# Kernel optimization log

Measured on AMD Instinct MI355X. Metric: run time of the kernel, lower is better.

Reference implementation:

```python
import jax, jax.numpy as jnp
import numpy as np

RATIO = 128        # compress_ratio (coff=1, no overlap)
HEAD_DIM = 512
RD = 64            # rope_head_dim
BLOCK_SIZE = 8192  # token block size of paged KV cache
ENTRIES = 64       # entries per compressed-cache block (BLOCK_SIZE // RATIO)
NUM_BLOCKS = 4     # physical blocks in the paged cache
EPS = 1e-6


def setup_inputs() -> dict:
    key = jax.random.key(0)
    ks = jax.random.split(key, 6)
    B, S, D = 2, 8192, 4096
    x = jax.random.normal(ks[0], (B, S, D), jnp.float32)
    wkv = jax.random.normal(ks[1], (D, HEAD_DIM), jnp.float32) * 0.02
    wgate = jax.random.normal(ks[2], (D, HEAD_DIM), jnp.float32) * 0.02
    ape = jax.random.normal(ks[3], (RATIO, HEAD_DIM), jnp.float32)
    norm_weight = jnp.ones((HEAD_DIM,), jnp.float32)
    # rotary tables for positions 0..S-1 over RD//2 frequencies
    inv_freq = 1.0 / (10000.0 ** (jnp.arange(0, RD, 2, dtype=jnp.float32) / RD))
    ang = jnp.arange(S, dtype=jnp.float32)[:, None] * inv_freq[None, :]
    cos, sin = jnp.cos(ang), jnp.sin(ang)
    # one physical block per sequence (prefill from start_pos=0)
    block_offsets = jnp.arange(B, dtype=jnp.int32).reshape(B, 1)
    return {"x": x, "wkv": wkv, "wgate": wgate, "ape": ape,
            "norm_weight": norm_weight, "cos": cos, "sin": sin,
            "block_offsets": block_offsets}


def reference(x, wkv, wgate, ape, norm_weight, cos, sin, block_offsets):
    B, S, D = x.shape
    NC = S // RATIO  # compressed tokens per sequence
    # projections, then reshape into compression windows of RATIO tokens
    kv = jnp.einsum('bsd,dh->bsh', x, wkv).reshape(B, NC, RATIO, HEAD_DIM)
    sc = jnp.einsum('bsd,dh->bsh', x, wgate).reshape(B, NC, RATIO, HEAD_DIM)
    # score_kv: gate scores + absolute-position bias -> softmax over the window,
    # weighted sum pools RATIO tokens into one compressed entry per channel
    w = jax.nn.softmax(sc + ape[None, None], axis=2)        # [B, NC, RATIO, H]
    comp = jnp.sum(w * kv, axis=2)                          # [B, NC, H]
    # RMSNorm (fp32 accumulation)
    ms = jnp.mean(jnp.square(comp.astype(jnp.float32)), axis=-1, keepdims=True)
    comp = (comp.astype(jnp.float32) * jax.lax.rsqrt(ms + EPS)).astype(x.dtype) * norm_weight
    # RoPE on last RD dims at the window-start token position (start_pos+1-ratio)
    pos = jnp.arange(NC) * RATIO                            # [NC]
    c, s = cos[pos], sin[pos]                               # [NC, RD//2]
    rot = comp[..., -RD:].reshape(B, NC, RD // 2, 2)
    rr = rot[..., 0] * c - rot[..., 1] * s
    ri = rot[..., 0] * s + rot[..., 1] * c
    comp = jnp.concatenate(
        [comp[..., :-RD], jnp.stack([rr, ri], axis=-1).reshape(B, NC, RD)], axis=-1)
    # scatter compressed entries into the paged block cache
    cidx = jnp.arange(NC)
    blk = (cidx * RATIO) // BLOCK_SIZE                      # logical block index
    off = cidx % ENTRIES                                    # offset within block
    phys = block_offsets[:, blk].astype(jnp.int32)          # [B, NC]
    cache = jnp.zeros((NUM_BLOCKS, ENTRIES, HEAD_DIM), x.dtype)
    cache = cache.at[phys.reshape(-1), jnp.tile(off, B)].set(comp.reshape(-1, HEAD_DIM))
    return cache
```

## Files before the change

### kernel.cpp

```cpp
#include <hip/hip_runtime.h>
#include <hip/hip_bf16.h>
#include <stdint.h>

typedef __bf16 bf16x8 __attribute__((ext_vector_type(8)));
typedef float f32x4 __attribute__((ext_vector_type(4)));

#define RATIO   128
#define HEADDIM 512
#define RD      64
#define NCW     64
#define BATCH   2
#define SEQ     8192
#define DIM     4096

__device__ __forceinline__ void gload16(const void* g, void* l) {
  __builtin_amdgcn_global_load_lds(
      (__attribute__((address_space(1))) const void*)g,
      (__attribute__((address_space(3))) void*)l, 16, 0, 0);
}

__device__ __forceinline__ __bf16 cvt_bf16(float f) {
  __hip_bfloat16 h = __float2bfloat16(f);
  return *reinterpret_cast<__bf16*>(&h);
}

__global__ __launch_bounds__(256) void prep_weights(
    const float* __restrict__ w0, const float* __restrict__ w1,
    __hip_bfloat16* __restrict__ wTs) {
  __shared__ float tile[64][132];
  const int wsel = blockIdx.z, hb = blockIdx.y, k0t = blockIdx.x;
  const float* in = wsel ? w1 : w0;
  const int t = threadIdx.x;
  const int h4 = (t & 31) * 4;
  #pragma unroll
  for (int p = 0; p < 8; ++p) {
    const int k = (t >> 5) + p * 8;
    const f32x4 v = *reinterpret_cast<const f32x4*>(
        in + (size_t)(k0t * 64 + k) * HEADDIM + hb * 128 + h4);
    tile[k][h4 + 0] = v[0]; tile[k][h4 + 1] = v[1];
    tile[k][h4 + 2] = v[2]; tile[k][h4 + 3] = v[3];
  }
  __syncthreads();
  const int row = t >> 1;
  __hip_bfloat16* outbase =
      wTs + (((size_t)(wsel * 4 + hb) * 64 + k0t) * 1024 + (size_t)row * 8) * 8;
  #pragma unroll
  for (int q = 0; q < 4; ++q) {
    const int slot = (t & 1) * 4 + q;
    const int kk = (slot ^ (row & 7)) * 8;
    bf16x8 c;
    #pragma unroll
    for (int j = 0; j < 8; ++j) c[j] = cvt_bf16(tile[kk + j][row]);
    *reinterpret_cast<bf16x8*>(outbase + slot * 8) = c;
  }
}

__device__ __forceinline__ bf16x8 ldfrag(const __hip_bfloat16* s, int row, int c16) {
  return *reinterpret_cast<const bf16x8*>(
      reinterpret_cast<const char*>(s) + row * 128 + ((c16 ^ (row & 7)) << 4));
}

__global__ __launch_bounds__(256, 2) void gemm_pool_kernel(
    const float* __restrict__ x,
    const __hip_bfloat16* __restrict__ wTs,
    const float* __restrict__ ape,
    float* __restrict__ comp) {
  __shared__ __hip_bfloat16 sA [128 * 64];
  __shared__ __hip_bfloat16 sKV[128 * 64];
  __shared__ __hip_bfloat16 sSC[128 * 64];
  __shared__ float red[3][2][128];

  const int u    = blockIdx.x;
  const int xcd  = u & 7;
  const int slot = u >> 3;
  const int win  = xcd + 8 * (slot >> 2);
  const int hb   = slot & 3;
  const int b    = win >> 6;
  const int nc   = win & 63;

  const int tid  = threadIdx.x;
  const int lane = tid & 63;
  const int wid  = tid >> 6;
  const int wm   = wid >> 1, wn = wid & 1;

  const float* xw = x + ((size_t)b * SEQ + (size_t)nc * RATIO) * DIM;
  const __hip_bfloat16* kvTiles = wTs + ((size_t)(0 * 4 + hb) * 64) * 8192;
  const __hip_bfloat16* scTiles = wTs + ((size_t)(1 * 4 + hb) * 64) * 8192;

  f32x4 acc_kv[4][4], acc_sc[4][4];
  #pragma unroll
  for (int i = 0; i < 4; ++i)
    #pragma unroll
    for (int j = 0; j < 4; ++j) {
      acc_kv[i][j] = {0.f, 0.f, 0.f, 0.f};
      acc_sc[i][j] = {0.f, 0.f, 0.f, 0.f};
    }

  const int r0   = tid >> 2;
  const int cb   = (tid & 3) * 16;
  const int c16b = (tid & 3) * 2;

  for (int k0t = 0; k0t < 64; ++k0t) {
    const int k0 = k0t * 64;
    __syncthreads();
    #pragma unroll
    for (int i = 0; i < 4; ++i) {
      const int ch = wid * 256 + i * 64;
      gload16(kvTiles + ((size_t)k0t * 1024 + ch + lane) * 8,
              (char*)sKV + ch * 16);
      gload16(scTiles + ((size_t)k0t * 1024 + ch + lane) * 8,
              (char*)sSC + ch * 16);
    }
    #pragma unroll
    for (int half = 0; half < 2; ++half) {
      const int r = r0 + half * 64;
      const f32x4* src = reinterpret_cast<const f32x4*>(xw + (size_t)r * DIM + k0 + cb);
      f32x4 v0 = src[0], v1 = src[1], v2 = src[2], v3 = src[3];
      bf16x8 a0, a1;
      #pragma unroll
      for (int j = 0; j < 4; ++j) {
        a0[j] = cvt_bf16(v0[j]); a0[4 + j] = cvt_bf16(v1[j]);
        a1[j] = cvt_bf16(v2[j]); a1[4 + j] = cvt_bf16(v3[j]);
      }
      char* abase = (char*)sA + r * 128;
      *reinterpret_cast<bf16x8*>(abase + ((c16b ^ (r & 7)) << 4)) = a0;
      *reinterpret_cast<bf16x8*>(abase + (((c16b + 1) ^ (r & 7)) << 4)) = a1;
    }
    asm volatile("s_waitcnt vmcnt(0)" ::: "memory");
    __syncthreads();

    #pragma unroll
    for (int s = 0; s < 2; ++s) {
      const int c16 = s * 4 + (lane >> 4);
      bf16x8 af[4];
      #pragma unroll
      for (int mt = 0; mt < 4; ++mt)
        af[mt] = ldfrag(sA, wm * 64 + mt * 16 + (lane & 15), c16);
      #pragma unroll
      for (int nt = 0; nt < 4; ++nt) {
        const int brow = wn * 64 + nt * 16 + (lane & 15);
        const bf16x8 bkv = ldfrag(sKV, brow, c16);
        const bf16x8 bsc = ldfrag(sSC, brow, c16);
        #pragma unroll
        for (int mt = 0; mt < 4; ++mt) {
          acc_kv[mt][nt] = __builtin_amdgcn_mfma_f32_16x16x32_bf16(af[mt], bkv, acc_kv[mt][nt], 0, 0, 0);
          acc_sc[mt][nt] = __builtin_amdgcn_mfma_f32_16x16x32_bf16(af[mt], bsc, acc_sc[mt][nt], 0, 0, 0);
        }
      }
    }
  }

  const int cl = lane & 15;
  const int g4 = (lane >> 4) * 4;

  #pragma unroll
  for (int nt = 0; nt < 4; ++nt) {
    const int h = hb * 128 + wn * 64 + nt * 16 + cl;
    #pragma unroll
    for (int mt = 0; mt < 4; ++mt) {
      const int rbase = wm * 64 + mt * 16 + g4;
      #pragma unroll
      for (int r = 0; r < 4; ++r)
        acc_sc[mt][nt][r] += ape[(size_t)(rbase + r) * HEADDIM + h];
    }
  }

  float mx[4];
  #pragma unroll
  for (int nt = 0; nt < 4; ++nt) {
    float m = -3.0e38f;
    #pragma unroll
    for (int mt = 0; mt < 4; ++mt)
      #pragma unroll
      for (int r = 0; r < 4; ++r) m = fmaxf(m, acc_sc[mt][nt][r]);
    m = fmaxf(m, __shfl_xor(m, 16));
    m = fmaxf(m, __shfl_xor(m, 32));
    mx[nt] = m;
  }
  if (lane < 16) {
    #pragma unroll
    for (int nt = 0; nt < 4; ++nt)
      red[0][wm][wn * 64 + nt * 16 + lane] = mx[nt];
  }
  __syncthreads();
  #pragma unroll
  for (int nt = 0; nt < 4; ++nt) {
    const int idx = wn * 64 + nt * 16 + cl;
    mx[nt] = fmaxf(red[0][0][idx], red[0][1][idx]);
  }

  float den[4], num[4];
  #pragma unroll
  for (int nt = 0; nt < 4; ++nt) {
    float d = 0.f, n = 0.f;
    #pragma unroll
    for (int mt = 0; mt < 4; ++mt)
      #pragma unroll
      for (int r = 0; r < 4; ++r) {
        const float e = __expf(acc_sc[mt][nt][r] - mx[nt]);
        d += e;
        n += e * acc_kv[mt][nt][r];
      }
    d += __shfl_xor(d, 16); d += __shfl_xor(d, 32);
    n += __shfl_xor(n, 16); n += __shfl_xor(n, 32);
    den[nt] = d; num[nt] = n;
  }
  if (lane < 16) {
    #pragma unroll
    for (int nt = 0; nt < 4; ++nt) {
      const int idx = wn * 64 + nt * 16 + lane;
      red[1][wm][idx] = den[nt];
      red[2][wm][idx] = num[nt];
    }
  }
  __syncthreads();
  if (wm == 0 && lane < 16) {
    #pragma unroll
    for (int nt = 0; nt < 4; ++nt) {
      const int idx = wn * 64 + nt * 16 + lane;
      const float dt = red[1][0][idx] + red[1][1][idx];
      const float nu = red[2][0][idx] + red[2][1][idx];
      comp[((size_t)b * NCW + nc) * HEADDIM + hb * 128 + idx] = nu / dt;
    }
  }
}

__global__ __launch_bounds__(64) void finalize_kernel(
    const float* __restrict__ comp,
    const float* __restrict__ nw,
    const float* __restrict__ cosg,
    const float* __restrict__ sing,
    const int* __restrict__ bo,
    float* __restrict__ out) {
  const int win = blockIdx.x;
  const int b = win >> 6, nc = win & 63;
  const int t = threadIdx.x;
  const float* cw = comp + (size_t)win * HEADDIM;

  float v[8];
  float ss = 0.f;
  #pragma unroll
  for (int j = 0; j < 8; ++j) { v[j] = cw[t * 8 + j]; ss += v[j] * v[j]; }
  #pragma unroll
  for (int o = 32; o; o >>= 1) ss += __shfl_xor(ss, o);
  const float scale = rsqrtf(ss / 512.0f + 1e-6f);

  float w[8];
  #pragma unroll
  for (int j = 0; j < 8; ++j) w[j] = v[j] * scale * nw[t * 8 + j];

  const int phys = bo[b];
  float* op = out + ((size_t)phys * NCW + nc) * HEADDIM + t * 8;
  if (t * 8 < HEADDIM - RD) {
    #pragma unroll
    for (int j = 0; j < 8; ++j) op[j] = w[j];
  } else {
    const int pos = nc * RATIO;
    #pragma unroll
    for (int j = 0; j < 8; j += 2) {
      const int i = (t * 8 + j - (HEADDIM - RD)) >> 1;
      const float co = cosg[(size_t)pos * 32 + i];
      const float si = sing[(size_t)pos * 32 + i];
      op[j]     = w[j] * co - w[j + 1] * si;
      op[j + 1] = w[j] * si + w[j + 1] * co;
    }
  }
}

extern "C" void kernel_launch(void* const* d_in, const int* in_sizes, int n_in,
                              void* d_out, int out_size, void* d_ws, size_t ws_size,
                              hipStream_t stream) {
  const float* x     = (const float*)d_in[0];
  const float* wkv   = (const float*)d_in[1];
  const float* wgate = (const float*)d_in[2];
  const float* ape   = (const float*)d_in[3];
  const float* nw    = (const float*)d_in[4];
  const float* cosg  = (const float*)d_in[5];
  const float* sing  = (const float*)d_in[6];
  const int*   bo    = (const int*)d_in[7];
  float* out = (float*)d_out;

  __hip_bfloat16* wTs = (__hip_bfloat16*)d_ws;
  float* comp = (float*)((char*)d_ws + (size_t)2 * HEADDIM * DIM * sizeof(__hip_bfloat16));

  (void)hipMemsetAsync(d_out, 0, (size_t)out_size * sizeof(float), stream);
  prep_weights<<<dim3(64, 4, 2), 256, 0, stream>>>(wkv, wgate, wTs);
  gemm_pool_kernel<<<dim3(512), 256, 0, stream>>>(x, wTs, ape, comp);
  finalize_kernel<<<dim3(128), 64, 0, stream>>>(comp, nw, cosg, sing, bo, out);
}
```

Baseline: 177.4 us.

## Interleave kv/gate weights, use 256-row tiles with double-buffered LDS pipeline

Measured after the change: 252.5 us. +42.4%, slower.

```diff
diff --git a/kernel.cpp b/kernel.cpp
--- a/kernel.cpp
+++ b/kernel.cpp
@@ -27,201 +27,177 @@
 __global__ __launch_bounds__(256) void prep_weights(
     const float* __restrict__ w0, const float* __restrict__ w1,
     __hip_bfloat16* __restrict__ wTs) {
-  __shared__ float tile[64][132];
-  const int wsel = blockIdx.z, hb = blockIdx.y, k0t = blockIdx.x;
-  const float* in = wsel ? w1 : w0;
-  const int t = threadIdx.x;
-  const int h4 = (t & 31) * 4;
-  #pragma unroll
-  for (int p = 0; p < 8; ++p) {
-    const int k = (t >> 5) + p * 8;
-    const f32x4 v = *reinterpret_cast<const f32x4*>(
-        in + (size_t)(k0t * 64 + k) * HEADDIM + hb * 128 + h4);
-    tile[k][h4 + 0] = v[0]; tile[k][h4 + 1] = v[1];
-    tile[k][h4 + 2] = v[2]; tile[k][h4 + 3] = v[3];
+  __shared__ float tile[2][64][128];
+  const int k0t = blockIdx.x;
+  const int j   = blockIdx.y;
+  const int t   = threadIdx.x;
+  const int kk  = t >> 5;
+  const int c4  = (t & 31) * 4;
+  #pragma unroll
+  for (int tensor = 0; tensor < 2; ++tensor) {
+    const float* in = tensor ? w1 : w0;
+    #pragma unroll
+    for (int p = 0; p < 8; ++p) {
+      const int k = p * 8 + kk;
+      const f32x4 v = *reinterpret_cast<const f32x4*>(
+          in + (size_t)(k0t * 64 + k) * HEADDIM + j * 128 + c4);
+      tile[tensor][k][c4 + 0] = v[0]; tile[tensor][k][c4 + 1] = v[1];
+      tile[tensor][k][c4 + 2] = v[2]; tile[tensor][k][c4 + 3] = v[3];
+    }
   }
   __syncthreads();
-  const int row = t >> 1;
-  __hip_bfloat16* outbase =
-      wTs + (((size_t)(wsel * 4 + hb) * 64 + k0t) * 1024 + (size_t)row * 8) * 8;
-  #pragma unroll
-  for (int q = 0; q < 4; ++q) {
-    const int slot = (t & 1) * 4 + q;
-    const int kk = (slot ^ (row & 7)) * 8;
+  const int row    = t;
+  const int chloc  = (row >> 4) * 8 + (row & 7);
+  const int tensor = (row >> 3) & 1;
+  __hip_bfloat16* ob = wTs + (((size_t)j * 64 + k0t) * 2048 + (size_t)row * 8) * 8;
+  #pragma unroll
+  for (int slot = 0; slot < 8; ++slot) {
+    const int k8 = (slot ^ (row & 7)) * 8;
     bf16x8 c;
     #pragma unroll
-    for (int j = 0; j < 8; ++j) c[j] = cvt_bf16(tile[kk + j][row]);
-    *reinterpret_cast<bf16x8*>(outbase + slot * 8) = c;
-  }
-}
-
-__device__ __forceinline__ bf16x8 ldfrag(const __hip_bfloat16* s, int row, int c16) {
-  return *reinterpret_cast<const bf16x8*>(
-      reinterpret_cast<const char*>(s) + row * 128 + ((c16 ^ (row & 7)) << 4));
-}
-
-__global__ __launch_bounds__(256, 2) void gemm_pool_kernel(
+    for (int jj = 0; jj < 8; ++jj) c[jj] = cvt_bf16(tile[tensor][k8 + jj][chloc]);
+    *reinterpret_cast<bf16x8*>(ob + slot * 8) = c;
+  }
+}
+
+__global__ __launch_bounds__(512, 2) void gemm_pool_kernel(
     const float* __restrict__ x,
     const __hip_bfloat16* __restrict__ wTs,
     const float* __restrict__ ape,
     float* __restrict__ comp) {
-  __shared__ __hip_bfloat16 sA [128 * 64];
-  __shared__ __hip_bfloat16 sKV[128 * 64];
-  __shared__ __hip_bfloat16 sSC[128 * 64];
-  __shared__ float red[3][2][128];
-
-  const int u    = blockIdx.x;
-  const int xcd  = u & 7;
-  const int slot = u >> 3;
-  const int win  = xcd + 8 * (slot >> 2);
-  const int hb   = slot & 3;
-  const int b    = win >> 6;
-  const int nc   = win & 63;
-
+  __shared__ char smem[131072];
+
+  const int u      = blockIdx.x;
+  const int rowblk = u & 63;
+  const int colblk = u >> 6;
   const int tid  = threadIdx.x;
   const int lane = tid & 63;
   const int wid  = tid >> 6;
-  const int wm   = wid >> 1, wn = wid & 1;
-
-  const float* xw = x + ((size_t)b * SEQ + (size_t)nc * RATIO) * DIM;
-  const __hip_bfloat16* kvTiles = wTs + ((size_t)(0 * 4 + hb) * 64) * 8192;
-  const __hip_bfloat16* scTiles = wTs + ((size_t)(1 * 4 + hb) * 64) * 8192;
-
-  f32x4 acc_kv[4][4], acc_sc[4][4];
-  #pragma unroll
-  for (int i = 0; i < 4; ++i)
-    #pragma unroll
-    for (int j = 0; j < 4; ++j) {
-      acc_kv[i][j] = {0.f, 0.f, 0.f, 0.f};
-      acc_sc[i][j] = {0.f, 0.f, 0.f, 0.f};
-    }
-
-  const int r0   = tid >> 2;
-  const int cb   = (tid & 3) * 16;
-  const int c16b = (tid & 3) * 2;
-
-  for (int k0t = 0; k0t < 64; ++k0t) {
-    const int k0 = k0t * 64;
-    __syncthreads();
+  const int wm   = wid >> 2, wn = wid & 3;
+
+  const float* xw = x + (size_t)rowblk * 256 * DIM;
+  const __hip_bfloat16* wsrc = wTs + (size_t)colblk * 64 * 2048 * 8;
+
+  const int arow  = tid >> 1;
+  const int ahalf = tid & 1;
+  const float* aBase = xw + (size_t)arow * DIM + ahalf * 32;
+
+  f32x4 acc[8][4];
+  #pragma unroll
+  for (int i = 0; i < 8; ++i)
+    #pragma unroll
+    for (int j = 0; j < 4; ++j) acc[i][j] = {0.f, 0.f, 0.f, 0.f};
+
+  auto issueA = [&](int k0t, f32x4* pv) {
+    const f32x4* s = reinterpret_cast<const f32x4*>(aBase + k0t * 64);
+    #pragma unroll
+    for (int q = 0; q < 8; ++q) pv[q] = s[q];
+  };
+  auto issueB = [&](int k0t, char* bufB) {
     #pragma unroll
     for (int i = 0; i < 4; ++i) {
       const int ch = wid * 256 + i * 64;
-      gload16(kvTiles + ((size_t)k0t * 1024 + ch + lane) * 8,
-              (char*)sKV + ch * 16);
-      gload16(scTiles + ((size_t)k0t * 1024 + ch + lane) * 8,
-              (char*)sSC + ch * 16);
-    }
-    #pragma unroll
-    for (int half = 0; half < 2; ++half) {
-      const int r = r0 + half * 64;
-      const f32x4* src = reinterpret_cast<const f32x4*>(xw + (size_t)r * DIM + k0 + cb);
-      f32x4 v0 = src[0], v1 = src[1], v2 = src[2], v3 = src[3];
-      bf16x8 a0, a1;
-      #pragma unroll
-      for (int j = 0; j < 4; ++j) {
-        a0[j] = cvt_bf16(v0[j]); a0[4 + j] = cvt_bf16(v1[j]);
-        a1[j] = cvt_bf16(v2[j]); a1[4 + j] = cvt_bf16(v3[j]);
-      }
-      char* abase = (char*)sA + r * 128;
-      *reinterpret_cast<bf16x8*>(abase + ((c16b ^ (r & 7)) << 4)) = a0;
-      *reinterpret_cast<bf16x8*>(abase + (((c16b + 1) ^ (r & 7)) << 4)) = a1;
-    }
-    asm volatile("s_waitcnt vmcnt(0)" ::: "memory");
-    __syncthreads();
-
+      gload16(wsrc + ((size_t)k0t * 2048 + ch + lane) * 8, bufB + ch * 16);
+    }
+  };
+  auto writeA = [&](char* bufA, const f32x4* pv) {
+    char* ab = bufA + arow * 128;
+    #pragma unroll
+    for (int q = 0; q < 4; ++q) {
+      bf16x8 c;
+      #pragma unroll
+      for (int jj = 0; jj < 4; ++jj) {
+        c[jj]     = cvt_bf16(pv[2 * q][jj]);
+        c[4 + jj] = cvt_bf16(pv[2 * q + 1][jj]);
+      }
+      *reinterpret_cast<bf16x8*>(ab + (((ahalf * 4 + q) ^ (arow & 7)) << 4)) = c;
+    }
+  };
+  auto compute = [&](const char* bufA, const char* bufB) {
     #pragma unroll
     for (int s = 0; s < 2; ++s) {
       const int c16 = s * 4 + (lane >> 4);
-      bf16x8 af[4];
-      #pragma unroll
-      for (int mt = 0; mt < 4; ++mt)
-        af[mt] = ldfrag(sA, wm * 64 + mt * 16 + (lane & 15), c16);
+      bf16x8 af[8];
+      #pragma unroll
+      for (int mt = 0; mt < 8; ++mt) {
+        const int r = wm * 128 + mt * 16 + (lane & 15);
+        af[mt] = *reinterpret_cast<const bf16x8*>(bufA + r * 128 + ((c16 ^ (r & 7)) << 4));
+      }
       #pragma unroll
       for (int nt = 0; nt < 4; ++nt) {
-        const int brow = wn * 64 + nt * 16 + (lane & 15);
-        const bf16x8 bkv = ldfrag(sKV, brow, c16);
-        const bf16x8 bsc = ldfrag(sSC, brow, c16);
+        const int cc = wn * 64 + nt * 16 + (lane & 15);
+        const bf16x8 bf = *reinterpret_cast<const bf16x8*>(bufB + cc * 128 + ((c16 ^ (cc & 7)) << 4));
         #pragma unroll
-        for (int mt = 0; mt < 4; ++mt) {
-          acc_kv[mt][nt] = __builtin_amdgcn_mfma_f32_16x16x32_bf16(af[mt], bkv, acc_kv[mt][nt], 0, 0, 0);
-          acc_sc[mt][nt] = __builtin_amdgcn_mfma_f32_16x16x32_bf16(af[mt], bsc, acc_sc[mt][nt], 0, 0, 0);
+        for (int mt = 0; mt < 8; ++mt)
+          acc[mt][nt] = __builtin_amdgcn_mfma_f32_16x16x32_bf16(af[mt], bf, acc[mt][nt], 0, 0, 0);
+      }
+    }
+  };
+
+  {
+    f32x4 pv[8];
+    issueA(0, pv);
+    issueB(0, smem + 32768);
+    asm volatile("s_waitcnt vmcnt(0)" ::: "memory");
+    writeA(smem, pv);
+  }
+  __syncthreads();
+
+  int cur = 0;
+  for (int t = 0; t < 64; ++t) {
+    char* A  = smem + cur * 65536;
+    char* B  = A + 32768;
+    char* An = smem + (cur ^ 1) * 65536;
+    char* Bn = An + 32768;
+    f32x4 nv[8];
+    if (t < 63) {
+      issueA(t + 1, nv);
+      issueB(t + 1, Bn);
+    }
+    compute(A, B);
+    if (t < 63) {
+      asm volatile("s_waitcnt vmcnt(0)" ::: "memory");
+      writeA(An, nv);
+    }
+    __syncthreads();
+    cur ^= 1;
+  }
+
+  const int win = rowblk * 2 + wm;
+  #pragma unroll
+  for (int nt = 0; nt < 4; ++nt) {
+    const int f  = wn * 4 + nt;
+    const int ch = colblk * 128 + f * 8 + (lane & 7);
+    if (lane & 8) {
+      #pragma unroll
+      for (int mt = 0; mt < 8; ++mt)
+        #pragma unroll
+        for (int r = 0; r < 4; ++r) {
+          const int rw = mt * 16 + ((lane >> 4) & 3) * 4 + r;
+          acc[mt][nt][r] += ape[(size_t)rw * HEADDIM + ch];
         }
-      }
-    }
-  }
-
-  const int cl = lane & 15;
-  const int g4 = (lane >> 4) * 4;
-
-  #pragma unroll
-  for (int nt = 0; nt < 4; ++nt) {
-    const int h = hb * 128 + wn * 64 + nt * 16 + cl;
-    #pragma unroll
-    for (int mt = 0; mt < 4; ++mt) {
-      const int rbase = wm * 64 + mt * 16 + g4;
-      #pragma unroll
-      for (int r = 0; r < 4; ++r)
-        acc_sc[mt][nt][r] += ape[(size_t)(rbase + r) * HEADDIM + h];
-    }
-  }
-
-  float mx[4];
-  #pragma unroll
-  for (int nt = 0; nt < 4; ++nt) {
+    }
     float m = -3.0e38f;
     #pragma unroll
-    for (int mt = 0; mt < 4; ++mt)
-      #pragma unroll
-      for (int r = 0; r < 4; ++r) m = fmaxf(m, acc_sc[mt][nt][r]);
+    for (int mt = 0; mt < 8; ++mt)
+      #pragma unroll
+      for (int r = 0; r < 4; ++r) m = fmaxf(m, acc[mt][nt][r]);
     m = fmaxf(m, __shfl_xor(m, 16));
     m = fmaxf(m, __shfl_xor(m, 32));
-    mx[nt] = m;
-  }
-  if (lane < 16) {
-    #pragma unroll
-    for (int nt = 0; nt < 4; ++nt)
-      red[0][wm][wn * 64 + nt * 16 + lane] = mx[nt];
-  }
-  __syncthreads();
-  #pragma unroll
-  for (int nt = 0; nt < 4; ++nt) {
-    const int idx = wn * 64 + nt * 16 + cl;
-    mx[nt] = fmaxf(red[0][0][idx], red[0][1][idx]);
-  }
-
-  float den[4], num[4];
-  #pragma unroll
-  for (int nt = 0; nt < 4; ++nt) {
-    float d = 0.f, n = 0.f;
-    #pragma unroll
-    for (int mt = 0; mt < 4; ++mt)
+    float den = 0.f, num = 0.f;
+    #pragma unroll
+    for (int mt = 0; mt < 8; ++mt)
       #pragma unroll
       for (int r = 0; r < 4; ++r) {
-        const float e = __expf(acc_sc[mt][nt][r] - mx[nt]);
-        d += e;
-        n += e * acc_kv[mt][nt][r];
-      }
-    d += __shfl_xor(d, 16); d += __shfl_xor(d, 32);
-    n += __shfl_xor(n, 16); n += __shfl_xor(n, 32);
-    den[nt] = d; num[nt] = n;
-  }
-  if (lane < 16) {
-    #pragma unroll
-    for (int nt = 0; nt < 4; ++nt) {
-      const int idx = wn * 64 + nt * 16 + lane;
-      red[1][wm][idx] = den[nt];
-      red[2][wm][idx] = num[nt];
-    }
-  }
-  __syncthreads();
-  if (wm == 0 && lane < 16) {
-    #pragma unroll
-    for (int nt = 0; nt < 4; ++nt) {
-      const int idx = wn * 64 + nt * 16 + lane;
-      const float dt = red[1][0][idx] + red[1][1][idx];
-      const float nu = red[2][0][idx] + red[2][1][idx];
-      comp[((size_t)b * NCW + nc) * HEADDIM + hb * 128 + idx] = nu / dt;
-    }
+        const float other = __shfl_xor(acc[mt][nt][r], 8);
+        const float e = __expf(acc[mt][nt][r] - m);
+        den += e;
+        num += e * other;
+      }
+    den += __shfl_xor(den, 16); den += __shfl_xor(den, 32);
+    num += __shfl_xor(num, 16); num += __shfl_xor(num, 32);
+    if ((lane & 8) && (lane < 16))
+      comp[(size_t)win * HEADDIM + ch] = num / den;
   }
 }
 
@@ -281,10 +257,10 @@
   float* out = (float*)d_out;
 
   __hip_bfloat16* wTs = (__hip_bfloat16*)d_ws;
-  float* comp = (float*)((char*)d_ws + (size_t)2 * HEADDIM * DIM * sizeof(__hip_bfloat16));
+  float* comp = (float*)((char*)d_ws + (size_t)8 * 1024 * 1024);
 
   (void)hipMemsetAsync(d_out, 0, (size_t)out_size * sizeof(float), stream);
-  prep_weights<<<dim3(64, 4, 2), 256, 0, stream>>>(wkv, wgate, wTs);
-  gemm_pool_kernel<<<dim3(512), 256, 0, stream>>>(x, wTs, ape, comp);
+  prep_weights<<<dim3(64, 4), 256, 0, stream>>>(wkv, wgate, wTs);
+  gemm_pool_kernel<<<dim3(256), 512, 0, stream>>>(x, wTs, ape, comp);
   finalize_kernel<<<dim3(128), 64, 0, stream>>>(comp, nw, cosg, sing, bo, out);
 }
```

## Double-buffer weight tiles in LDS and prefetch activation tile into registers

Applied to the files above, without the earlier changes.

Result: slower. 209.6 us (+18.2%).

```diff
diff --git a/kernel.cpp b/kernel.cpp
--- a/kernel.cpp
+++ b/kernel.cpp
@@ -12,6 +12,9 @@
 #define BATCH   2
 #define SEQ     8192
 #define DIM     4096
+
+#define SBAR() __builtin_amdgcn_sched_barrier(0)
+#define BARR() __builtin_amdgcn_s_barrier()
 
 __device__ __forceinline__ void gload16(const void* g, void* l) {
   __builtin_amdgcn_global_load_lds(
@@ -55,9 +58,8 @@
   }
 }
 
-__device__ __forceinline__ bf16x8 ldfrag(const __hip_bfloat16* s, int row, int c16) {
-  return *reinterpret_cast<const bf16x8*>(
-      reinterpret_cast<const char*>(s) + row * 128 + ((c16 ^ (row & 7)) << 4));
+__device__ __forceinline__ bf16x8 ldfrag(const char* s, int row, int c16) {
+  return *reinterpret_cast<const bf16x8*>(s + row * 128 + ((c16 ^ (row & 7)) << 4));
 }
 
 __global__ __launch_bounds__(256, 2) void gemm_pool_kernel(
@@ -65,10 +67,8 @@
     const __hip_bfloat16* __restrict__ wTs,
     const float* __restrict__ ape,
     float* __restrict__ comp) {
-  __shared__ __hip_bfloat16 sA [128 * 64];
-  __shared__ __hip_bfloat16 sKV[128 * 64];
-  __shared__ __hip_bfloat16 sSC[128 * 64];
-  __shared__ float red[3][2][128];
+  __shared__ char smem[81920];
+  char* sA = smem;
 
   const int u    = blockIdx.x;
   const int xcd  = u & 7;
@@ -96,39 +96,37 @@
       acc_sc[i][j] = {0.f, 0.f, 0.f, 0.f};
     }
 
-  const int r0   = tid >> 2;
-  const int cb   = (tid & 3) * 16;
-  const int c16b = (tid & 3) * 2;
-
-  for (int k0t = 0; k0t < 64; ++k0t) {
-    const int k0 = k0t * 64;
-    __syncthreads();
+  const int arow  = tid >> 1;
+  const int ahalf = tid & 1;
+  const float* aBase = xw + (size_t)arow * DIM + ahalf * 32;
+
+  auto issueA = [&](int k0t, f32x4* pv) {
+    const f32x4* s = reinterpret_cast<const f32x4*>(aBase + k0t * 64);
+    #pragma unroll
+    for (int q = 0; q < 8; ++q) pv[q] = s[q];
+  };
+  auto issueB = [&](int k0t, char* bKV, char* bSC) {
     #pragma unroll
     for (int i = 0; i < 4; ++i) {
       const int ch = wid * 256 + i * 64;
-      gload16(kvTiles + ((size_t)k0t * 1024 + ch + lane) * 8,
-              (char*)sKV + ch * 16);
-      gload16(scTiles + ((size_t)k0t * 1024 + ch + lane) * 8,
-              (char*)sSC + ch * 16);
-    }
-    #pragma unroll
-    for (int half = 0; half < 2; ++half) {
-      const int r = r0 + half * 64;
-      const f32x4* src = reinterpret_cast<const f32x4*>(xw + (size_t)r * DIM + k0 + cb);
-      f32x4 v0 = src[0], v1 = src[1], v2 = src[2], v3 = src[3];
-      bf16x8 a0, a1;
-      #pragma unroll
-      for (int j = 0; j < 4; ++j) {
-        a0[j] = cvt_bf16(v0[j]); a0[4 + j] = cvt_bf16(v1[j]);
-        a1[j] = cvt_bf16(v2[j]); a1[4 + j] = cvt_bf16(v3[j]);
+      gload16(kvTiles + ((size_t)k0t * 1024 + ch + lane) * 8, bKV + ch * 16);
+      gload16(scTiles + ((size_t)k0t * 1024 + ch + lane) * 8, bSC + ch * 16);
+    }
+  };
+  auto writeA = [&](const f32x4* pv) {
+    char* ab = sA + arow * 128;
+    #pragma unroll
+    for (int q = 0; q < 4; ++q) {
+      bf16x8 c;
+      #pragma unroll
+      for (int jj = 0; jj < 4; ++jj) {
+        c[jj]     = cvt_bf16(pv[2 * q][jj]);
+        c[4 + jj] = cvt_bf16(pv[2 * q + 1][jj]);
       }
-      char* abase = (char*)sA + r * 128;
-      *reinterpret_cast<bf16x8*>(abase + ((c16b ^ (r & 7)) << 4)) = a0;
-      *reinterpret_cast<bf16x8*>(abase + (((c16b + 1) ^ (r & 7)) << 4)) = a1;
-    }
-    asm volatile("s_waitcnt vmcnt(0)" ::: "memory");
-    __syncthreads();
-
+      *reinterpret_cast<bf16x8*>(ab + (((ahalf * 4 + q) ^ (arow & 7)) << 4)) = c;
+    }
+  };
+  auto compute = [&](const char* bKV, const char* bSC) {
     #pragma unroll
     for (int s = 0; s < 2; ++s) {
       const int c16 = s * 4 + (lane >> 4);
@@ -139,8 +137,8 @@
       #pragma unroll
       for (int nt = 0; nt < 4; ++nt) {
         const int brow = wn * 64 + nt * 16 + (lane & 15);
-        const bf16x8 bkv = ldfrag(sKV, brow, c16);
-        const bf16x8 bsc = ldfrag(sSC, brow, c16);
+        const bf16x8 bkv = ldfrag(bKV, brow, c16);
+        const bf16x8 bsc = ldfrag(bSC, brow, c16);
         #pragma unroll
         for (int mt = 0; mt < 4; ++mt) {
           acc_kv[mt][nt] = __builtin_amdgcn_mfma_f32_16x16x32_bf16(af[mt], bkv, acc_kv[mt][nt], 0, 0, 0);
@@ -148,8 +146,37 @@
         }
       }
     }
-  }
-
+  };
+
+  {
+    f32x4 pv[8];
+    issueA(0, pv);
+    issueB(0, smem + 16384, smem + 49152);
+    writeA(pv);
+  }
+  __syncthreads();
+
+  for (int t = 0; t < 64; ++t) {
+    const int cur = t & 1;
+    char* bKV  = smem + 16384 + cur * 16384;
+    char* bSC  = smem + 49152 + cur * 16384;
+    char* bKVn = smem + 16384 + (cur ^ 1) * 16384;
+    char* bSCn = smem + 49152 + (cur ^ 1) * 16384;
+    const bool pf = (t < 63);
+    f32x4 nv[8];
+    if (pf) {
+      issueB(t + 1, bKVn, bSCn);
+      issueA(t + 1, nv);
+      SBAR();
+    }
+    compute(bKV, bSC);
+    BARR(); SBAR();
+    if (pf) writeA(nv);
+    __syncthreads();
+  }
+
+  float* redp = (float*)smem;
+  auto RED = [&](int a, int b2, int c) -> float& { return redp[(a * 2 + b2) * 128 + c]; };
   const int cl = lane & 15;
   const int g4 = (lane >> 4) * 4;
 
@@ -180,14 +207,15 @@
   if (lane < 16) {
     #pragma unroll
     for (int nt = 0; nt < 4; ++nt)
-      red[0][wm][wn * 64 + nt * 16 + lane] = mx[nt];
+      RED(0, wm, wn * 64 + nt * 16 + lane) = mx[nt];
   }
   __syncthreads();
   #pragma unroll
   for (int nt = 0; nt < 4; ++nt) {
     const int idx = wn * 64 + nt * 16 + cl;
-    mx[nt] = fmaxf(red[0][0][idx], red[0][1][idx]);
-  }
+    mx[nt] = fmaxf(RED(0, 0, idx), RED(0, 1, idx));
+  }
+  __syncthreads();
 
   float den[4], num[4];
   #pragma unroll
@@ -209,8 +237,8 @@
     #pragma unroll
     for (int nt = 0; nt < 4; ++nt) {
       const int idx = wn * 64 + nt * 16 + lane;
-      red[1][wm][idx] = den[nt];
-      red[2][wm][idx] = num[nt];
+      RED(1, wm, idx) = den[nt];
+      RED(2, wm, idx) = num[nt];
     }
   }
   __syncthreads();
@@ -218,8 +246,8 @@
     #pragma unroll
     for (int nt = 0; nt < 4; ++nt) {
       const int idx = wn * 64 + nt * 16 + lane;
-      const float dt = red[1][0][idx] + red[1][1][idx];
-      const float nu = red[2][0][idx] + red[2][1][idx];
+      const float dt = RED(1, 0, idx) + RED(1, 1, idx);
+      const float nu = RED(2, 0, idx) + RED(2, 1, idx);
       comp[((size_t)b * NCW + nc) * HEADDIM + hb * 128 + idx] = nu / dt;
     }
   }
@@ -281,7 +309,7 @@
   float* out = (float*)d_out;
 
   __hip_bfloat16* wTs = (__hip_bfloat16*)d_ws;
-  float* comp = (float*)((char*)d_ws + (size_t)2 * HEADDIM * DIM * sizeof(__hip_bfloat16));
+  float* comp = (float*)((char*)d_ws + (size_t)8 * 1024 * 1024);
 
   (void)hipMemsetAsync(d_out, 0, (size_t)out_size * sizeof(float), stream);
   prep_weights<<<dim3(64, 4, 2), 256, 0, stream>>>(wkv, wgate, wTs);
```
